# Performance work log

Hardware: AMD Instinct MI355X
Metric: run time of the kernel (lower is better)

The kernel has to match this reference:

```python
import jax, jax.numpy as jnp
import numpy as np
from jax import lax

N_NODES = 100000
N_EDGES = 600000  # even: edges stored as consecutive reverse pairs
NODE_F = 64
EDGE_F = 16
EDGE_H = 128
NODE_H = 128
NUM_STEPS = 6


def setup_inputs() -> dict:
    key = jax.random.key(0)
    ks = jax.random.split(key, 16)
    # paired reverse edges: edge 2k is (src,dst), edge 2k+1 is (dst,src)
    src = jax.random.randint(ks[0], (N_EDGES // 2,), 0, N_NODES, dtype=jnp.int32)
    dst = jax.random.randint(ks[1], (N_EDGES // 2,), 0, N_NODES, dtype=jnp.int32)
    from_nodes = jnp.stack([src, dst], axis=1).reshape(-1)
    to_nodes = jnp.stack([dst, src], axis=1).reshape(-1)
    edges = jnp.stack([from_nodes, to_nodes], axis=0)
    return {
        "node_features": jax.random.normal(ks[2], (N_NODES, NODE_F), jnp.float32),
        "edge_features": jax.random.normal(ks[3], (N_EDGES, EDGE_F), jnp.float32),
        "edge_hiddens": jnp.zeros((N_EDGES, EDGE_H), jnp.float32),
        "edges": edges,
        "W1_w": jax.random.normal(ks[4], (NODE_F, EDGE_H), jnp.float32) / np.sqrt(NODE_F),
        "W1_b": jnp.zeros((EDGE_H,), jnp.float32),
        "W2_w": jax.random.normal(ks[5], (EDGE_F, EDGE_H), jnp.float32) / np.sqrt(EDGE_F),
        "W2_b": jnp.zeros((EDGE_H,), jnp.float32),
        "W3_w": jax.random.normal(ks[6], (EDGE_H, EDGE_H), jnp.float32) / np.sqrt(EDGE_H),
        "W3_b": jnp.zeros((EDGE_H,), jnp.float32),
        "U1_w": jax.random.normal(ks[7], (NODE_F, NODE_H), jnp.float32) / np.sqrt(NODE_F),
        "U1_b": jnp.zeros((NODE_H,), jnp.float32),
        "U2_w": jax.random.normal(ks[8], (EDGE_H, NODE_H), jnp.float32) / np.sqrt(EDGE_H),
        "U2_b": jnp.zeros((NODE_H,), jnp.float32),
    }


def reference(node_features, edge_features, edge_hiddens, edges,
              W1_w, W1_b, W2_w, W2_b, W3_w, W3_b, U1_w, U1_b, U2_w, U2_b):
    from_nodes = edges[0]
    to_nodes = edges[1]
    n_edges = edges.shape[1]
    # backlink of edge i is its reverse pair: even i -> i+1, odd i -> i-1
    idx = jnp.arange(n_edges)
    backlink = idx + ((idx + 1) % 2) * 2 - 1

    # loop-invariant terms
    W1_x_u = (node_features @ W1_w + W1_b)[from_nodes]     # [E, EH]
    W2_x_uv = edge_features @ W2_w + W2_b                  # [E, EH]

    def step(h, _):
        # sum edge hiddens by source node, gather back per-edge, drop backlink
        s = jax.ops.segment_sum(h, from_nodes, num_segments=N_NODES)  # [N, EH]
        wu = s[from_nodes] - h[backlink]                               # [E, EH]
        h_new = jax.nn.relu(W1_x_u + W2_x_uv + (wu @ W3_w + W3_b))
        return h_new, None

    edge_h, _ = lax.scan(step, edge_hiddens, None, length=NUM_STEPS)

    U1_x_u = node_features @ U1_w + U1_b                   # [N, NH]
    U2_vu = edge_h @ U2_w + U2_b                           # [E, NH]
    agg = jax.ops.segment_sum(U2_vu, to_nodes, num_segments=N_NODES)
    node_hiddens = jax.nn.relu(U1_x_u + agg)               # [N, NH]
    return node_hiddens
```

## Files before the change

### kernel.cpp

```cpp
#include <hip/hip_runtime.h>
#include <hip/hip_bf16.h>

#define N_NODES 100000
#define N_EDGES 600000
#define SCAN_BLOCKS ((N_NODES + 255) / 256)

typedef __bf16 bf16;
typedef __bf16 bf16x2 __attribute__((ext_vector_type(2)));
typedef __bf16 bf16x4 __attribute__((ext_vector_type(4)));
typedef __bf16 bf16x8 __attribute__((ext_vector_type(8)));
typedef float f32x4 __attribute__((ext_vector_type(4)));

__global__ void deg_hist(const int* __restrict__ from, int* __restrict__ deg, int E) {
    int e = blockIdx.x * blockDim.x + threadIdx.x;
    if (e < E) atomicAdd(&deg[from[e]], 1);
}

__global__ __launch_bounds__(256) void block_sums(
    const int* __restrict__ deg, int* __restrict__ bsum)
{
    __shared__ int s[256];
    int i = blockIdx.x * 256 + threadIdx.x;
    s[threadIdx.x] = (i < N_NODES) ? deg[i] : 0;
    __syncthreads();
    for (int st = 128; st > 0; st >>= 1) {
        if (threadIdx.x < st) s[threadIdx.x] += s[threadIdx.x + st];
        __syncthreads();
    }
    if (threadIdx.x == 0) bsum[blockIdx.x] = s[0];
}

__global__ __launch_bounds__(256) void scan_partials(
    const int* __restrict__ bsum, int* __restrict__ bpref, int* __restrict__ off)
{
    __shared__ int s[SCAN_BLOCKS];
    for (int i = threadIdx.x; i < SCAN_BLOCKS; i += 256) s[i] = bsum[i];
    __syncthreads();
    if (threadIdx.x == 0) {
        int run = 0;
        for (int i = 0; i < SCAN_BLOCKS; i++) { int t = s[i]; s[i] = run; run += t; }
        off[N_NODES] = run;
    }
    __syncthreads();
    for (int i = threadIdx.x; i < SCAN_BLOCKS; i += 256) bpref[i] = s[i];
}

__global__ __launch_bounds__(256) void block_scan(
    const int* __restrict__ deg, const int* __restrict__ bpref,
    int* __restrict__ off, int* __restrict__ cursor)
{
    __shared__ int s[256];
    int i = blockIdx.x * 256 + threadIdx.x;
    int v = (i < N_NODES) ? deg[i] : 0;
    s[threadIdx.x] = v;
    __syncthreads();
    for (int st = 1; st < 256; st <<= 1) {
        int x = (threadIdx.x >= st) ? s[threadIdx.x - st] : 0;
        __syncthreads();
        s[threadIdx.x] += x;
        __syncthreads();
    }
    if (i < N_NODES) {
        int o = bpref[blockIdx.x] + s[threadIdx.x] - v;
        off[i] = o;
        cursor[i] = o;
    }
}

__global__ void scatter_csr(const int* __restrict__ from, int* __restrict__ cursor,
                            int* __restrict__ se, int* __restrict__ rank, int E) {
    int e = blockIdx.x * blockDim.x + threadIdx.x;
    if (e < E) {
        int p = atomicAdd(&cursor[from[e]], 1);
        se[p] = e;
        rank[e] = p;
    }
}

__global__ void make_maps(const int* __restrict__ se, const int* __restrict__ from,
                          const int* __restrict__ rank,
                          int* __restrict__ fromP, int* __restrict__ backP, int E) {
    int i = blockIdx.x * blockDim.x + threadIdx.x;
    if (i < E) {
        int e = se[i];
        fromP[i] = from[e];
        backP[i] = rank[e ^ 1];
    }
}

__global__ __launch_bounds__(256) void node_gemm(
    const float* __restrict__ A, const float* __restrict__ B,
    const float* __restrict__ bias, float* __restrict__ C, int M)
{
    __shared__ float As[16][65];
    __shared__ float Bs[16][128];
    int row0 = blockIdx.x * 64;
    int tid = threadIdx.x;
    int tx = tid & 15, ty = tid >> 4;
    float acc[4][8];
    #pragma unroll
    for (int i = 0; i < 4; i++)
        #pragma unroll
        for (int j = 0; j < 8; j++) acc[i][j] = 0.f;

    for (int kk = 0; kk < 64; kk += 16) {
        int m  = tid >> 2;
        int k4 = (tid & 3) * 4;
        float4 v = make_float4(0.f, 0.f, 0.f, 0.f);
        if (row0 + m < M)
            v = *(const float4*)(A + (size_t)(row0 + m) * 64 + kk + k4);
        As[k4 + 0][m] = v.x; As[k4 + 1][m] = v.y;
        As[k4 + 2][m] = v.z; As[k4 + 3][m] = v.w;
        #pragma unroll
        for (int t = 0; t < 2; t++) {
            int id = tid + t * 256;
            int k = id >> 5, n4 = (id & 31) * 4;
            *(float4*)(&Bs[k][n4]) = *(const float4*)(B + (size_t)(kk + k) * 128 + n4);
        }
        __syncthreads();
        #pragma unroll
        for (int k = 0; k < 16; k++) {
            float a[4], b[8];
            #pragma unroll
            for (int i = 0; i < 4; i++) a[i] = As[k][ty * 4 + i];
            #pragma unroll
            for (int j = 0; j < 8; j++) b[j] = Bs[k][tx + j * 16];
            #pragma unroll
            for (int i = 0; i < 4; i++)
                #pragma unroll
                for (int j = 0; j < 8; j++) acc[i][j] += a[i] * b[j];
        }
        __syncthreads();
    }
    #pragma unroll
    for (int i = 0; i < 4; i++) {
        int r = row0 + ty * 4 + i;
        if (r < M) {
            #pragma unroll
            for (int j = 0; j < 8; j++) {
                int c = tx + j * 16;
                C[(size_t)r * 128 + c] = acc[i][j] + bias[c];
            }
        }
    }
}

__global__ __launch_bounds__(256) void base_sorted(
    const float* __restrict__ nodeW1, const int* __restrict__ fromP,
    const int* __restrict__ se, const float* __restrict__ ef,
    const float* __restrict__ W2, const float* __restrict__ W2b,
    const float* __restrict__ W3b, bf16* __restrict__ baseP)
{
    int tid = threadIdx.x;
    int c0 = (tid & 31) * 4;
    int sub = tid >> 5;
    float4 w[16];
    #pragma unroll
    for (int k = 0; k < 16; k++) w[k] = *(const float4*)(W2 + k * 128 + c0);
    float4 bias;
    {
        float4 a = *(const float4*)(W2b + c0);
        float4 b = *(const float4*)(W3b + c0);
        bias = make_float4(a.x + b.x, a.y + b.y, a.z + b.z, a.w + b.w);
    }
    #pragma unroll 1
    for (int it = 0; it < 64; ++it) {
        int i = blockIdx.x * 512 + it * 8 + sub;
        if (i >= N_EDGES) break;
        const float* efr = ef + (size_t)se[i] * 16;
        float4 nv = *(const float4*)(nodeW1 + (size_t)fromP[i] * 128 + c0);
        float4 acc = make_float4(bias.x + nv.x, bias.y + nv.y,
                                 bias.z + nv.z, bias.w + nv.w);
        #pragma unroll
        for (int k = 0; k < 16; k++) {
            float s = efr[k];
            acc.x += s * w[k].x; acc.y += s * w[k].y;
            acc.z += s * w[k].z; acc.w += s * w[k].w;
        }
        bf16x4 o;
        o[0] = (bf16)acc.x; o[1] = (bf16)acc.y; o[2] = (bf16)acc.z; o[3] = (bf16)acc.w;
        *(bf16x4*)(baseP + (size_t)i * 128 + c0) = o;
    }
}

__global__ __launch_bounds__(256) void prep_weights(
    const float* __restrict__ W3, const float* __restrict__ U2,
    bf16* __restrict__ W3T, bf16* __restrict__ U2T)
{
    int i = blockIdx.x * 256 + threadIdx.x;
    if (i < 128 * 128) {
        int k = i >> 7, n = i & 127;
        W3T[n * 128 + k] = (bf16)W3[k * 128 + n];
        U2T[n * 128 + k] = (bf16)U2[k * 128 + n];
    }
}

__global__ __launch_bounds__(256) void edge_mfma_v2(
    const bf16* __restrict__ baseP, const bf16* __restrict__ gin,
    const bf16* __restrict__ S, const int* __restrict__ fromP,
    const int* __restrict__ backP, const bf16* __restrict__ BT,
    bf16* __restrict__ gout, int fused)
{
    __shared__ bf16 Bsw[128 * 128];
    int tid = threadIdx.x;

    #pragma unroll
    for (int t = 0; t < 8; t++) {
        int c = tid + t * 256;
        int cmr = c & 15;
        int cq  = (c >> 4) & 3;
        int ckt = (c >> 6) & 3;
        int cn  = c >> 8;
        int brow = cn * 16 + cmr;
        int bcol = ckt * 32 + cq * 8;
        *(bf16x8*)&Bsw[(size_t)c * 8] =
            *(const bf16x8*)(BT + (size_t)brow * 128 + bcol);
    }
    __syncthreads();

    int wave = tid >> 6, lane = tid & 63;
    int quad = lane >> 4, mr = lane & 15;

    #pragma unroll 1
    for (int it = 0; it < 4; ++it) {
        int i0 = blockIdx.x * 256 + wave * 64 + it * 16;
        if (i0 >= N_EDGES) break;
        int i = i0 + mr;

        bf16x8 afr[4];
        if (!fused) {
            #pragma unroll
            for (int kt = 0; kt < 4; kt++) {
                bf16x8 bb = *(const bf16x8*)(baseP + (size_t)i * 128 + kt * 32 + quad * 8);
                #pragma unroll
                for (int j = 0; j < 8; j++)
                    afr[kt][j] = (bf16)fmaxf((float)bb[j], 0.f);
            }
        } else {
            const bf16* sr = S   + (size_t)fromP[i] * 128;
            const bf16* gr = gin + (size_t)backP[i] * 128;
            #pragma unroll
            for (int kt = 0; kt < 4; kt++) {
                int c = kt * 32 + quad * 8;
                bf16x8 bb = *(const bf16x8*)(baseP + (size_t)i * 128 + c);
                bf16x8 gg = *(const bf16x8*)(gr + c);
                bf16x8 ss = *(const bf16x8*)(sr + c);
                #pragma unroll
                for (int j = 0; j < 8; j++) {
                    float v = (float)bb[j] + (float)ss[j] - (float)gg[j];
                    afr[kt][j] = (bf16)fmaxf(v, 0.f);
                }
            }
        }

        f32x4 acc[8];
        #pragma unroll
        for (int n = 0; n < 8; n++) acc[n] = (f32x4){0.f, 0.f, 0.f, 0.f};
        #pragma unroll
        for (int kt = 0; kt < 4; kt++) {
            #pragma unroll
            for (int n = 0; n < 8; n++) {
                bf16x8 b = *(const bf16x8*)&Bsw[(size_t)(((n * 4 + kt) * 64) + lane) * 8];
                acc[n] = __builtin_amdgcn_mfma_f32_16x16x32_bf16(afr[kt], b, acc[n], 0, 0, 0);
            }
        }

        #pragma unroll
        for (int np = 0; np < 4; np++) {
            int n0 = np * 2;
            #pragma unroll
            for (int reg = 0; reg < 4; reg++) {
                float v0 = acc[n0][reg], v1 = acc[n0 + 1][reg];
                float o0 = __shfl_xor(v0, 1);
                float o1 = __shfl_xor(v1, 1);
                bf16x2 pk;
                int colb;
                if ((mr & 1) == 0) {
                    pk[0] = (bf16)v0; pk[1] = (bf16)o0;
                    colb = n0 * 16 + mr;
                } else {
                    pk[0] = (bf16)o1; pk[1] = (bf16)v1;
                    colb = (n0 + 1) * 16 + (mr ^ 1);
                }
                int row = i0 + quad * 4 + reg;
                *(bf16x2*)(gout + (size_t)row * 128 + colb) = pk;
            }
        }
    }
}

__global__ __launch_bounds__(256) void segsum_stream(
    const bf16* __restrict__ g, const int* __restrict__ off, bf16* __restrict__ S)
{
    int n = blockIdx.x * 4 + (threadIdx.x >> 6);
    if (n >= N_NODES) return;
    int lane = threadIdx.x & 63;
    int o0 = off[n], o1 = off[n + 1];
    float a0 = 0.f, a1 = 0.f;
    for (int i = o0; i < o1; ++i) {
        bf16x2 v = *(const bf16x2*)(g + (size_t)i * 128 + lane * 2);
        a0 += (float)v[0];
        a1 += (float)v[1];
    }
    bf16x2 o; o[0] = (bf16)a0; o[1] = (bf16)a1;
    *(bf16x2*)(S + (size_t)n * 128 + lane * 2) = o;
}

__global__ __launch_bounds__(256) void segsum_final(
    const bf16* __restrict__ g, const int* __restrict__ off,
    const int* __restrict__ backP, float* __restrict__ agg)
{
    int n = blockIdx.x * 4 + (threadIdx.x >> 6);
    if (n >= N_NODES) return;
    int lane = threadIdx.x & 63;
    int o0 = off[n], o1 = off[n + 1];
    float a0 = 0.f, a1 = 0.f;
    for (int i = o0; i < o1; ++i) {
        int e = backP[i];
        bf16x2 v = *(const bf16x2*)(g + (size_t)e * 128 + lane * 2);
        a0 += (float)v[0];
        a1 += (float)v[1];
    }
    *(float2*)(agg + (size_t)n * 128 + lane * 2) = make_float2(a0, a1);
}

__global__ __launch_bounds__(256) void final_out(
    const float* __restrict__ U1x, const float* __restrict__ agg,
    const int* __restrict__ deg, const float* __restrict__ U2b,
    float* __restrict__ out)
{
    int gid = blockIdx.x * 256 + threadIdx.x;
    int n  = gid >> 5;
    if (n >= N_NODES) return;
    int c4 = gid & 31;
    float d = (float)deg[n];
    float4 a  = *(const float4*)(U1x + (size_t)n * 128 + c4 * 4);
    float4 ag = *(const float4*)(agg + (size_t)n * 128 + c4 * 4);
    float4 ub = *(const float4*)(U2b + c4 * 4);
    float4 r;
    r.x = fmaxf(a.x + ag.x + d * ub.x, 0.f);
    r.y = fmaxf(a.y + ag.y + d * ub.y, 0.f);
    r.z = fmaxf(a.z + ag.z + d * ub.z, 0.f);
    r.w = fmaxf(a.w + ag.w + d * ub.w, 0.f);
    *(float4*)(out + (size_t)n * 128 + c4 * 4) = r;
}

extern "C" void kernel_launch(void* const* d_in, const int* in_sizes, int n_in,
                              void* d_out, int out_size, void* d_ws, size_t ws_size,
                              hipStream_t stream) {
    const float* nf  = (const float*)d_in[0];
    const float* ef  = (const float*)d_in[1];
    const int* edges = (const int*)d_in[3];
    const int* from  = edges;
    const float* W1w = (const float*)d_in[4];
    const float* W1b = (const float*)d_in[5];
    const float* W2w = (const float*)d_in[6];
    const float* W2b = (const float*)d_in[7];
    const float* W3w = (const float*)d_in[8];
    const float* W3b = (const float*)d_in[9];
    const float* U1w = (const float*)d_in[10];
    const float* U1b = (const float*)d_in[11];
    const float* U2w = (const float*)d_in[12];
    const float* U2b = (const float*)d_in[13];
    float* out = (float*)d_out;

    const size_t NODE_MAT = (size_t)N_NODES * 128;
    const size_t EDGE_MAT = (size_t)N_EDGES * 128;
    char* w = (char*)d_ws;
    float* nodeW1 = (float*)w; w += NODE_MAT * 4;
    float* agg    = (float*)w; w += NODE_MAT * 4;
    bf16*  S      = (bf16*)w;  w += NODE_MAT * 2;
    bf16*  baseP  = (bf16*)w;  w += EDGE_MAT * 2;
    bf16*  g0     = (bf16*)w;  w += EDGE_MAT * 2;
    bf16*  g1     = (bf16*)w;  w += EDGE_MAT * 2;
    bf16*  W3T    = (bf16*)w;  w += 128 * 128 * 2;
    bf16*  U2T    = (bf16*)w;  w += 128 * 128 * 2;
    int*   deg    = (int*)w;   w += (size_t)N_NODES * 4;
    int*   off    = (int*)w;   w += (size_t)(N_NODES + 1) * 4;
    int*   cursor = (int*)w;   w += (size_t)N_NODES * 4;
    int*   bsum   = (int*)w;   w += (size_t)SCAN_BLOCKS * 4;
    int*   bpref  = (int*)w;   w += (size_t)SCAN_BLOCKS * 4;
    int*   se     = (int*)w;   w += (size_t)N_EDGES * 4;
    int*   rank   = (int*)w;   w += (size_t)N_EDGES * 4;
    int*   fromP  = (int*)w;   w += (size_t)N_EDGES * 4;
    int*   backP  = (int*)w;   w += (size_t)N_EDGES * 4;

    hipMemsetAsync(deg, 0, (size_t)N_NODES * 4, stream);
    deg_hist<<<(N_EDGES + 255) / 256, 256, 0, stream>>>(from, deg, N_EDGES);
    block_sums<<<SCAN_BLOCKS, 256, 0, stream>>>(deg, bsum);
    scan_partials<<<1, 256, 0, stream>>>(bsum, bpref, off);
    block_scan<<<SCAN_BLOCKS, 256, 0, stream>>>(deg, bpref, off, cursor);
    scatter_csr<<<(N_EDGES + 255) / 256, 256, 0, stream>>>(from, cursor, se, rank, N_EDGES);
    make_maps<<<(N_EDGES + 255) / 256, 256, 0, stream>>>(se, from, rank, fromP, backP, N_EDGES);

    prep_weights<<<(128 * 128 + 255) / 256, 256, 0, stream>>>(W3w, U2w, W3T, U2T);
    node_gemm<<<(N_NODES + 63) / 64, 256, 0, stream>>>(nf, W1w, W1b, nodeW1, N_NODES);
    base_sorted<<<(N_EDGES + 511) / 512, 256, 0, stream>>>(
        nodeW1, fromP, se, ef, W2w, W2b, W3b, baseP);

    const int EGRID = (N_EDGES + 255) / 256;
    bf16* G[2] = {g0, g1};
    edge_mfma_v2<<<EGRID, 256, 0, stream>>>(
        baseP, G[0], S, fromP, backP, W3T, G[0], 0);
    segsum_stream<<<(N_NODES + 3) / 4, 256, 0, stream>>>(G[0], off, S);
    int cur = 0;
    for (int it = 1; it < 5; ++it) {
        edge_mfma_v2<<<EGRID, 256, 0, stream>>>(
            baseP, G[cur], S, fromP, backP, W3T, G[cur ^ 1], 1);
        cur ^= 1;
        segsum_stream<<<(N_NODES + 3) / 4, 256, 0, stream>>>(G[cur], off, S);
    }
    edge_mfma_v2<<<EGRID, 256, 0, stream>>>(
        baseP, G[cur], S, fromP, backP, U2T, G[cur ^ 1], 1);
    cur ^= 1;
    segsum_final<<<(N_NODES + 3) / 4, 256, 0, stream>>>(G[cur], off, backP, agg);

    node_gemm<<<(N_NODES + 63) / 64, 256, 0, stream>>>(nf, U1w, U1b, nodeW1, N_NODES);
    final_out<<<(N_NODES * 32 + 255) / 256, 256, 0, stream>>>(nodeW1, agg, deg, U2b, out);
}
```

Before: 1.655 ms.

## Write backlink-permuted copy in edge kernel to avoid gathered backlink reads

The edge MFMA kernel now writes each output row twice: once in sorted order for the segment sum, and once scattered to its backlink position. The next step can then read the backlink term contiguously instead of gathering it through backP. The final step reads the scattered copy directly and so drops its gather. The segment-sum kernels are merged into one template that has two half-waves handle alternate edges with 4-wide loads. The cost is an extra scattered write and an extra edge-sized buffer.

```diff
diff --git a/kernel.cpp b/kernel.cpp
--- a/kernel.cpp
+++ b/kernel.cpp
@@ -195,11 +195,11 @@
     }
 }
 
-__global__ __launch_bounds__(256) void edge_mfma_v2(
-    const bf16* __restrict__ baseP, const bf16* __restrict__ gin,
+__global__ __launch_bounds__(256) void edge_mfma_v3(
+    const bf16* __restrict__ baseP, const bf16* __restrict__ gback,
     const bf16* __restrict__ S, const int* __restrict__ fromP,
     const int* __restrict__ backP, const bf16* __restrict__ BT,
-    bf16* __restrict__ gout, int fused)
+    bf16* __restrict__ gsOut, bf16* __restrict__ gbOut, int fused)
 {
     __shared__ bf16 Bsw[128 * 128];
     int tid = threadIdx.x;
@@ -237,8 +237,8 @@
                     afr[kt][j] = (bf16)fmaxf((float)bb[j], 0.f);
             }
         } else {
-            const bf16* sr = S   + (size_t)fromP[i] * 128;
-            const bf16* gr = gin + (size_t)backP[i] * 128;
+            const bf16* sr = S     + (size_t)fromP[i] * 128;
+            const bf16* gr = gback + (size_t)i * 128;
             #pragma unroll
             for (int kt = 0; kt < 4; kt++) {
                 int c = kt * 32 + quad * 8;
@@ -265,6 +265,9 @@
             }
         }
 
+        int brow[4];
+        #pragma unroll
+        for (int reg = 0; reg < 4; reg++) brow[reg] = backP[i0 + quad * 4 + reg];
         #pragma unroll
         for (int np = 0; np < 4; np++) {
             int n0 = np * 2;
@@ -283,45 +286,41 @@
                     colb = (n0 + 1) * 16 + (mr ^ 1);
                 }
                 int row = i0 + quad * 4 + reg;
-                *(bf16x2*)(gout + (size_t)row * 128 + colb) = pk;
+                if (gsOut) *(bf16x2*)(gsOut + (size_t)row * 128 + colb) = pk;
+                *(bf16x2*)(gbOut + (size_t)brow[reg] * 128 + colb) = pk;
             }
         }
     }
 }
 
-__global__ __launch_bounds__(256) void segsum_stream(
-    const bf16* __restrict__ g, const int* __restrict__ off, bf16* __restrict__ S)
+template<int FP32OUT>
+__global__ __launch_bounds__(256) void segsum2(
+    const bf16* __restrict__ g, const int* __restrict__ off,
+    bf16* __restrict__ Sout, float* __restrict__ aggout)
 {
     int n = blockIdx.x * 4 + (threadIdx.x >> 6);
     if (n >= N_NODES) return;
     int lane = threadIdx.x & 63;
+    int half = lane >> 5;
+    int c0 = (lane & 31) * 4;
     int o0 = off[n], o1 = off[n + 1];
-    float a0 = 0.f, a1 = 0.f;
-    for (int i = o0; i < o1; ++i) {
-        bf16x2 v = *(const bf16x2*)(g + (size_t)i * 128 + lane * 2);
-        a0 += (float)v[0];
-        a1 += (float)v[1];
-    }
-    bf16x2 o; o[0] = (bf16)a0; o[1] = (bf16)a1;
-    *(bf16x2*)(S + (size_t)n * 128 + lane * 2) = o;
-}
-
-__global__ __launch_bounds__(256) void segsum_final(
-    const bf16* __restrict__ g, const int* __restrict__ off,
-    const int* __restrict__ backP, float* __restrict__ agg)
-{
-    int n = blockIdx.x * 4 + (threadIdx.x >> 6);
-    if (n >= N_NODES) return;
-    int lane = threadIdx.x & 63;
-    int o0 = off[n], o1 = off[n + 1];
-    float a0 = 0.f, a1 = 0.f;
-    for (int i = o0; i < o1; ++i) {
-        int e = backP[i];
-        bf16x2 v = *(const bf16x2*)(g + (size_t)e * 128 + lane * 2);
-        a0 += (float)v[0];
-        a1 += (float)v[1];
-    }
-    *(float2*)(agg + (size_t)n * 128 + lane * 2) = make_float2(a0, a1);
+    float a0 = 0.f, a1 = 0.f, a2 = 0.f, a3 = 0.f;
+    for (int i = o0 + half; i < o1; i += 2) {
+        bf16x4 v = *(const bf16x4*)(g + (size_t)i * 128 + c0);
+        a0 += (float)v[0]; a1 += (float)v[1];
+        a2 += (float)v[2]; a3 += (float)v[3];
+    }
+    a0 += __shfl_xor(a0, 32); a1 += __shfl_xor(a1, 32);
+    a2 += __shfl_xor(a2, 32); a3 += __shfl_xor(a3, 32);
+    if (half == 0) {
+        if (FP32OUT) {
+            *(float4*)(aggout + (size_t)n * 128 + c0) = make_float4(a0, a1, a2, a3);
+        } else {
+            bf16x4 o;
+            o[0] = (bf16)a0; o[1] = (bf16)a1; o[2] = (bf16)a2; o[3] = (bf16)a3;
+            *(bf16x4*)(Sout + (size_t)n * 128 + c0) = o;
+        }
+    }
 }
 
 __global__ __launch_bounds__(256) void final_out(
@@ -371,8 +370,9 @@
     float* agg    = (float*)w; w += NODE_MAT * 4;
     bf16*  S      = (bf16*)w;  w += NODE_MAT * 2;
     bf16*  baseP  = (bf16*)w;  w += EDGE_MAT * 2;
-    bf16*  g0     = (bf16*)w;  w += EDGE_MAT * 2;
-    bf16*  g1     = (bf16*)w;  w += EDGE_MAT * 2;
+    bf16*  gs     = (bf16*)w;  w += EDGE_MAT * 2;
+    bf16*  gbA    = (bf16*)w;  w += EDGE_MAT * 2;
+    bf16*  gbB    = (bf16*)w;  w += EDGE_MAT * 2;
     bf16*  W3T    = (bf16*)w;  w += 128 * 128 * 2;
     bf16*  U2T    = (bf16*)w;  w += 128 * 128 * 2;
     int*   deg    = (int*)w;   w += (size_t)N_NODES * 4;
@@ -399,21 +399,22 @@
         nodeW1, fromP, se, ef, W2w, W2b, W3b, baseP);
 
     const int EGRID = (N_EDGES + 255) / 256;
-    bf16* G[2] = {g0, g1};
-    edge_mfma_v2<<<EGRID, 256, 0, stream>>>(
-        baseP, G[0], S, fromP, backP, W3T, G[0], 0);
-    segsum_stream<<<(N_NODES + 3) / 4, 256, 0, stream>>>(G[0], off, S);
+    const int SGRID = (N_NODES + 3) / 4;
+    bf16* GB[2] = {gbA, gbB};
     int cur = 0;
+    edge_mfma_v3<<<EGRID, 256, 0, stream>>>(
+        baseP, GB[cur], S, fromP, backP, W3T, gs, GB[cur], 0);
+    segsum2<0><<<SGRID, 256, 0, stream>>>(gs, off, S, agg);
     for (int it = 1; it < 5; ++it) {
-        edge_mfma_v2<<<EGRID, 256, 0, stream>>>(
-            baseP, G[cur], S, fromP, backP, W3T, G[cur ^ 1], 1);
+        edge_mfma_v3<<<EGRID, 256, 0, stream>>>(
+            baseP, GB[cur], S, fromP, backP, W3T, gs, GB[cur ^ 1], 1);
         cur ^= 1;
-        segsum_stream<<<(N_NODES + 3) / 4, 256, 0, stream>>>(G[cur], off, S);
-    }
-    edge_mfma_v2<<<EGRID, 256, 0, stream>>>(
-        baseP, G[cur], S, fromP, backP, U2T, G[cur ^ 1], 1);
+        segsum2<0><<<SGRID, 256, 0, stream>>>(gs, off, S, agg);
+    }
+    edge_mfma_v3<<<EGRID, 256, 0, stream>>>(
+        baseP, GB[cur], S, fromP, backP, U2T, nullptr, GB[cur ^ 1], 1);
     cur ^= 1;
-    segsum_final<<<(N_NODES + 3) / 4, 256, 0, stream>>>(G[cur], off, backP, agg);
+    segsum2<1><<<SGRID, 256, 0, stream>>>(GB[cur], off, S, agg);
 
     node_gemm<<<(N_NODES + 63) / 64, 256, 0, stream>>>(nf, U1w, U1b, nodeW1, N_NODES);
     final_out<<<(N_NODES * 32 + 255) / 256, 256, 0, stream>>>(nodeW1, agg, deg, U2b, out);
```

Result: slower. 1.801 ms (+8.9%).
